# Optimization experiments

Measured on AMD Instinct MI355X. Metric: run time of the kernel, lower is better.

## Reference

```python
import jax, jax.numpy as jnp
import numpy as np

N_NODES = 100000
N_EDGES = 1600000
N_GRAPHS = 256
D = 128
L = 3
N_OUT = 10


def setup_inputs() -> dict:
    key = jax.random.key(0)
    ks = jax.random.split(key, 6)
    x = jax.random.normal(ks[0], (N_NODES, D), dtype=jnp.float32)
    edge_index = jax.random.randint(ks[1], (2, N_EDGES), 0, N_NODES, dtype=jnp.int64)
    batch = jnp.sort(jax.random.randint(ks[2], (N_NODES,), 0, N_GRAPHS, dtype=jnp.int64))
    conv_w = jax.random.normal(ks[3], (L, D, D), dtype=jnp.float32) * (1.0 / np.sqrt(D))
    conv_b = jnp.zeros((L, D), dtype=jnp.float32)
    out_w = jax.random.normal(ks[4], (3 * D, N_OUT), dtype=jnp.float32) * (1.0 / np.sqrt(3 * D))
    out_b = jnp.zeros((N_OUT,), dtype=jnp.float32)
    return {"x": x, "edge_index": edge_index, "batch": batch,
            "conv_w": conv_w, "conv_b": conv_b, "out_w": out_w, "out_b": out_b}


def reference(x, edge_index, batch, conv_w, conv_b, out_w, out_b):
    N = x.shape[0]
    # --- add self-loops (PyG GCNConv default) ---
    loop = jnp.arange(N, dtype=edge_index.dtype)
    src = jnp.concatenate([edge_index[0], loop])  # [E+N]
    dst = jnp.concatenate([edge_index[1], loop])
    # --- symmetric normalization: deg computed on dst (col) ---
    deg = jax.ops.segment_sum(jnp.ones_like(dst, dtype=x.dtype), dst, num_segments=N)
    dinv = jnp.where(deg > 0, jax.lax.rsqrt(jnp.maximum(deg, 1.0)), 0.0)
    norm = dinv[src] * dinv[dst]  # [E+N]

    h = x
    for l in range(conv_w.shape[0]):
        h = h @ conv_w[l]                                   # [N, D] transform first
        msg = h[src] * norm[:, None]                        # gather + scale
        h = jax.ops.segment_sum(msg, dst, num_segments=N)   # scatter-add
        h = jax.nn.relu(h + conv_b[l])

    # --- global max / mean / add pooling over graphs ---
    B = N_GRAPHS
    gmax = jax.ops.segment_max(h, batch, num_segments=B)
    gsum = jax.ops.segment_sum(h, batch, num_segments=B)
    cnt = jax.ops.segment_sum(jnp.ones((N, 1), h.dtype), batch, num_segments=B)
    gmean = gsum / jnp.maximum(cnt, 1.0)
    pooled = jnp.concatenate([gmax, gmean, gsum], axis=1)   # [B, 3D]
    # dropout p=0.5 is identity in eval mode
    return pooled @ out_w + out_b
```

## Files before the change

### kernel.cpp

```cpp
#include <hip/hip_runtime.h>
#include <hip/hip_bf16.h>

#define D 128
#define NP 8
#define DPB 64
#define KPB (DPB * NP)
#define SUB 64
#define CAP_SUB 64

typedef __attribute__((ext_vector_type(8))) __bf16 bf16x8;
typedef __attribute__((ext_vector_type(4))) float f32x4;
typedef __attribute__((ext_vector_type(4))) short s16x4;
typedef __attribute__((ext_vector_type(8))) short s16x8;

static __device__ __forceinline__ short f2bf(float f) {
    union { float f; unsigned u; } in; in.f = f;
    unsigned u = in.u;
    u += 0x7fffu + ((u >> 16) & 1u);
    return (short)(u >> 16);
}

__global__ void k_bucket(const int* __restrict__ src, const int* __restrict__ dst,
                         int* __restrict__ bcnt, int* __restrict__ staging,
                         int E, int KBE) {
    int i = blockIdx.x * 256 + threadIdx.x;
    if (i >= E) return;
    int d = dst[i], s = src[i];
    int b = d >> 6;
    int key = ((d & 63) << 3) | (s >> 14);
    int j = blockIdx.x & (SUB - 1);
    int slot = atomicAdd(&bcnt[j * KBE + b], 1);
    if (slot < CAP_SUB) staging[((size_t)j * KBE + b) * CAP_SUB + slot] = (key << 17) | s;
}

__global__ void k_btot(const int* __restrict__ bcnt, int* __restrict__ btot, int KBE) {
    int b = blockIdx.x * 256 + threadIdx.x;
    if (b >= KBE) return;
    int v = 0;
    #pragma unroll
    for (int j = 0; j < SUB; j++) {
        int c = bcnt[j * KBE + b];
        v += (c > CAP_SUB) ? CAP_SUB : c;
    }
    btot[b] = v;
}

__global__ void k_bscan(const int* __restrict__ btot, int* __restrict__ bbase,
                        int* __restrict__ row_ptr, int nkeys, int KBE) {
    __shared__ int sm[512];
    __shared__ int carry;
    int t = threadIdx.x;
    if (t == 0) carry = 0;
    __syncthreads();
    for (int c0 = 0; c0 < KBE; c0 += 512) {
        int b = c0 + t;
        int v = (b < KBE) ? btot[b] : 0;
        sm[t] = v;
        __syncthreads();
        for (int off = 1; off < 512; off <<= 1) {
            int x = (t >= off) ? sm[t - off] : 0;
            __syncthreads();
            sm[t] += x;
            __syncthreads();
        }
        if (b < KBE) bbase[b] = sm[t] - v + carry;
        __syncthreads();
        if (t == 0) carry += sm[511];
        __syncthreads();
    }
    if (t == 0) { bbase[KBE] = carry; row_ptr[nkeys] = carry; }
}

__global__ __launch_bounds__(256) void k_build(
    const int* __restrict__ staging, const int* __restrict__ bcnt,
    const int* __restrict__ bbase, int* __restrict__ row_ptr,
    int* __restrict__ csr_src, float* __restrict__ dinv, int N, int KBE)
{
    const int b = blockIdx.x;
    const int tid = threadIdx.x;
    __shared__ int cnt[KPB];
    __shared__ int subn[SUB];
    __shared__ int chunkbuf[256];
    __shared__ int carry;

    if (tid < SUB) {
        int c = bcnt[tid * KBE + b];
        subn[tid] = (c > CAP_SUB) ? CAP_SUB : c;
    }
    for (int k = tid; k < KPB; k += 256) cnt[k] = 0;
    if (tid == 0) carry = 0;
    __syncthreads();

    const int base = bbase[b];
    const int nb = bbase[b + 1] - base;
    const int j = tid >> 2, l4 = tid & 3;
    const int* __restrict__ sreg = staging + ((size_t)j * KBE + b) * CAP_SUB;
    const int sn = subn[j];

    for (int e = l4; e < sn; e += 4)
        atomicAdd(&cnt[sreg[e] >> 17], 1);
    __syncthreads();

    #pragma unroll 1
    for (int c = 0; c < KPB / 256; c++) {
        int idx = c * 256 + tid;
        int v = cnt[idx];
        chunkbuf[tid] = v;
        __syncthreads();
        for (int off = 1; off < 256; off <<= 1) {
            int x = (tid >= off) ? chunkbuf[tid - off] : 0;
            __syncthreads();
            chunkbuf[tid] += x;
            __syncthreads();
        }
        cnt[idx] = chunkbuf[tid] - v + carry;
        __syncthreads();
        if (tid == 255) carry += chunkbuf[255];
        __syncthreads();
    }

    for (int k = tid; k < KPB; k += 256)
        row_ptr[(size_t)b * KPB + k] = base + cnt[k];
    for (int dl = tid; dl < DPB; dl += 256) {
        int d = b * DPB + dl;
        if (d < N) {
            int hi2 = (dl == DPB - 1) ? nb : cnt[(dl + 1) * NP];
            int deg = hi2 - cnt[dl * NP];
            dinv[d] = rsqrtf((float)deg + 1.0f);
        }
    }
    __syncthreads();

    for (int e = l4; e < sn; e += 4) {
        int w = sreg[e];
        int slot = base + atomicAdd(&cnt[w >> 17], 1);
        csr_src[slot] = w & 0x1FFFF;
    }
}

__global__ void k_gseg(const int* __restrict__ batch, int* __restrict__ gstart,
                       int* __restrict__ gcnt, int N, int B) {
    int g = blockIdx.x * blockDim.x + threadIdx.x;
    if (g > B) return;
    int lo = 0, hi = N;
    while (lo < hi) {
        int mid = (lo + hi) >> 1;
        if (batch[mid] < g) lo = mid + 1; else hi = mid;
    }
    gstart[g] = lo;
    if (g < B) {
        int lo2 = lo, hi2 = N;
        while (lo2 < hi2) {
            int mid = (lo2 + hi2) >> 1;
            if (batch[mid] < g + 1) lo2 = mid + 1; else hi2 = mid;
        }
        gcnt[g] = lo2 - lo;
    }
}

__global__ void k_cvt_x(const float* __restrict__ x, const float* __restrict__ dinv,
                        short* __restrict__ xb, int total4) {
    int i = blockIdx.x * blockDim.x + threadIdx.x;
    if (i < total4) {
        float d = dinv[i >> 5];
        float4 v = ((const float4*)x)[i];
        s16x4 o;
        o.x = f2bf(v.x * d); o.y = f2bf(v.y * d);
        o.z = f2bf(v.z * d); o.w = f2bf(v.w * d);
        ((s16x4*)xb)[i] = o;
    }
}

__global__ void k_cvt_w(const float* __restrict__ W, short* __restrict__ Wt, int total) {
    int i = blockIdx.x * blockDim.x + threadIdx.x;
    if (i < total) {
        int l = i >> 14;
        int rem = i & 16383;
        int n = rem >> 7;
        int k = rem & 127;
        Wt[i] = f2bf(W[(l << 14) + (k << 7) + n]);
    }
}

__global__ __launch_bounds__(256) void k_layer(
    const short* __restrict__ hin, const int* __restrict__ row_ptr,
    const int* __restrict__ csr_src, const float* __restrict__ dinv,
    const short* __restrict__ Wt, const float* __restrict__ bias,
    short* __restrict__ hout, float* __restrict__ hrelu, int N, int mode)
{
    __shared__ __align__(16) short tile[16 * 128];
    const int tid = threadIdx.x;
    const int wave = tid >> 6;
    const int lane = tid & 63;
    const int group = lane >> 4;
    const int lg = lane & 15;
    const int off = lg * 8;
    const int node_base = blockIdx.x * 16;
    const int r = wave * 4 + group;
    const int i = node_base + r;

    short* dstp = &tile[r * 128 + ((lg ^ (r & 7)) << 3)];
    if (i < N) {
        float acc[8];
        bf16x8 v = *(const bf16x8*)(hin + (size_t)i * D + off);
        #pragma unroll
        for (int k = 0; k < 8; k++) acc[k] = (float)v[k];

        int t = row_ptr[i * NP];
        const int end = row_ptr[i * NP + NP];
        const int nfull = (end - t) >> 3;

        int i0, i1, i2, i3, i4, i5, i6, i7;
        if (nfull > 0) {
            i0 = csr_src[t + 0]; i1 = csr_src[t + 1];
            i2 = csr_src[t + 2]; i3 = csr_src[t + 3];
            i4 = csr_src[t + 4]; i5 = csr_src[t + 5];
            i6 = csr_src[t + 6]; i7 = csr_src[t + 7];
        }
        #pragma unroll 1
        for (int c = 0; c < nfull; c++) {
            bf16x8 v0 = *(const bf16x8*)(hin + (size_t)i0 * D + off);
            bf16x8 v1 = *(const bf16x8*)(hin + (size_t)i1 * D + off);
            bf16x8 v2 = *(const bf16x8*)(hin + (size_t)i2 * D + off);
            bf16x8 v3 = *(const bf16x8*)(hin + (size_t)i3 * D + off);
            bf16x8 v4 = *(const bf16x8*)(hin + (size_t)i4 * D + off);
            bf16x8 v5 = *(const bf16x8*)(hin + (size_t)i5 * D + off);
            bf16x8 v6 = *(const bf16x8*)(hin + (size_t)i6 * D + off);
            bf16x8 v7 = *(const bf16x8*)(hin + (size_t)i7 * D + off);
            t += 8;
            if (c + 1 < nfull) {
                i0 = csr_src[t + 0]; i1 = csr_src[t + 1];
                i2 = csr_src[t + 2]; i3 = csr_src[t + 3];
                i4 = csr_src[t + 4]; i5 = csr_src[t + 5];
                i6 = csr_src[t + 6]; i7 = csr_src[t + 7];
            }
            #pragma unroll
            for (int k = 0; k < 8; k++)
                acc[k] += ((((float)v0[k] + (float)v1[k]) + ((float)v2[k] + (float)v3[k]))
                         + (((float)v4[k] + (float)v5[k]) + ((float)v6[k] + (float)v7[k])));
        }
        for (; t + 4 <= end; t += 4) {
            int j0 = csr_src[t + 0], j1 = csr_src[t + 1];
            int j2 = csr_src[t + 2], j3 = csr_src[t + 3];
            bf16x8 v0 = *(const bf16x8*)(hin + (size_t)j0 * D + off);
            bf16x8 v1 = *(const bf16x8*)(hin + (size_t)j1 * D + off);
            bf16x8 v2 = *(const bf16x8*)(hin + (size_t)j2 * D + off);
            bf16x8 v3 = *(const bf16x8*)(hin + (size_t)j3 * D + off);
            #pragma unroll
            for (int k = 0; k < 8; k++)
                acc[k] += (((float)v0[k] + (float)v1[k]) + ((float)v2[k] + (float)v3[k]));
        }
        for (; t < end; t++) {
            int j0 = csr_src[t];
            bf16x8 v0 = *(const bf16x8*)(hin + (size_t)j0 * D + off);
            #pragma unroll
            for (int k = 0; k < 8; k++) acc[k] += (float)v0[k];
        }

        const float di = dinv[i];
        s16x8 o;
        #pragma unroll
        for (int k = 0; k < 8; k++) o[k] = f2bf(acc[k] * di);
        *(s16x8*)dstp = o;
    } else {
        s16x8 z = {0, 0, 0, 0, 0, 0, 0, 0};
        *(s16x8*)dstp = z;
    }
    __syncthreads();

    bf16x8 afrag[4];
    #pragma unroll
    for (int kt = 0; kt < 4; kt++)
        afrag[kt] = *(const bf16x8*)(&tile[lg * 128 + (((group + 4 * kt) ^ (lg & 7)) << 3)]);

    f32x4 acc2[2];
    #pragma unroll
    for (int nt = 0; nt < 2; nt++) { f32x4 z = {0.f, 0.f, 0.f, 0.f}; acc2[nt] = z; }
    #pragma unroll
    for (int nt = 0; nt < 2; nt++) {
        const short* bp = Wt + (size_t)(wave * 32 + nt * 16 + lg) * D + group * 8;
        #pragma unroll
        for (int kt = 0; kt < 4; kt++) {
            bf16x8 b = *(const bf16x8*)(bp + kt * 32);
            acc2[nt] = __builtin_amdgcn_mfma_f32_16x16x32_bf16(afrag[kt], b, acc2[nt], 0, 0, 0);
        }
    }

    float bcol[2];
    #pragma unroll
    for (int nt = 0; nt < 2; nt++) bcol[nt] = bias[wave * 32 + nt * 16 + lg];
    const int row0 = node_base + group * 4;
    #pragma unroll
    for (int i2 = 0; i2 < 4; i2++) {
        int r2 = row0 + i2;
        if (r2 < N) {
            if (mode == 0) {
                float dr = dinv[r2];
                #pragma unroll
                for (int nt = 0; nt < 2; nt++) {
                    int col = wave * 32 + nt * 16 + lg;
                    float val = fmaxf(acc2[nt][i2] + bcol[nt], 0.0f);
                    hout[(size_t)r2 * D + col] = f2bf(val * dr);
                }
            } else {
                #pragma unroll
                for (int nt = 0; nt < 2; nt++) {
                    int col = wave * 32 + nt * 16 + lg;
                    hrelu[(size_t)r2 * D + col] = fmaxf(acc2[nt][i2] + bcol[nt], 0.0f);
                }
            }
        }
    }
}

__global__ __launch_bounds__(256) void k_pool(const float* __restrict__ hrelu,
                                              const int* __restrict__ gstart,
                                              const int* __restrict__ gcnt,
                                              float* __restrict__ pmax,
                                              float* __restrict__ psum, int B) {
    int g = blockIdx.x >> 2;
    int q = blockIdx.x & 3;
    int c = threadIdx.x & 127;
    int p = threadIdx.x >> 7;
    int start = gstart[g];
    int endr = start + gcnt[g];

    float mx0 = 0.f, mx1 = 0.f, sm0 = 0.f, sm1 = 0.f;
    int r = start + q * 2 + p;
    for (; r + 8 < endr; r += 16) {
        float v0 = hrelu[(size_t)r * D + c];
        float v1 = hrelu[(size_t)(r + 8) * D + c];
        mx0 = fmaxf(mx0, v0); sm0 += v0;
        mx1 = fmaxf(mx1, v1); sm1 += v1;
    }
    if (r < endr) {
        float v0 = hrelu[(size_t)r * D + c];
        mx0 = fmaxf(mx0, v0); sm0 += v0;
    }
    float mx = fmaxf(mx0, mx1), sm = sm0 + sm1;

    __shared__ float smx[128], ssm[128];
    if (p == 1) { smx[c] = mx; ssm[c] = sm; }
    __syncthreads();
    if (p == 0) {
        pmax[((size_t)q * B + g) * D + c] = fmaxf(mx, smx[c]);
        psum[((size_t)q * B + g) * D + c] = sm + ssm[c];
    }
}

__global__ void k_final(const float* __restrict__ pmax, const float* __restrict__ psum,
                        const int* __restrict__ gcnt, const float* __restrict__ ow,
                        const float* __restrict__ ob, float* __restrict__ out, int B) {
    int g = blockIdx.x;
    int t = threadIdx.x;
    float part[10];
    #pragma unroll
    for (int o = 0; o < 10; o++) part[o] = 0.f;
    float invc = 1.0f / fmaxf((float)gcnt[g], 1.0f);
    for (int k = t; k < 3 * D; k += 64) {
        int c = (k < D) ? k : ((k < 2 * D) ? k - D : k - 2 * D);
        float pk;
        if (k < D) {
            float m = pmax[(size_t)g * D + c];
            #pragma unroll
            for (int q = 1; q < 4; q++) m = fmaxf(m, pmax[((size_t)q * B + g) * D + c]);
            pk = m;
        } else {
            float s = psum[(size_t)g * D + c];
            #pragma unroll
            for (int q = 1; q < 4; q++) s += psum[((size_t)q * B + g) * D + c];
            pk = (k < 2 * D) ? s * invc : s;
        }
        const float* w = ow + k * 10;
        #pragma unroll
        for (int o = 0; o < 10; o++) part[o] += pk * w[o];
    }
    #pragma unroll
    for (int off = 32; off > 0; off >>= 1)
        #pragma unroll
        for (int o = 0; o < 10; o++) part[o] += __shfl_down(part[o], off, 64);
    if (t == 0)
        #pragma unroll
        for (int o = 0; o < 10; o++) out[g * 10 + o] = part[o] + ob[o];
}

extern "C" void kernel_launch(void* const* d_in, const int* in_sizes, int n_in,
                              void* d_out, int out_size, void* d_ws, size_t ws_size,
                              hipStream_t stream) {
    const float* x     = (const float*)d_in[0];
    const int*   ei    = (const int*)d_in[1];
    const int*   batch = (const int*)d_in[2];
    const float* convw = (const float*)d_in[3];
    const float* convb = (const float*)d_in[4];
    const float* outw  = (const float*)d_in[5];
    const float* outb  = (const float*)d_in[6];
    float* out = (float*)d_out;

    const int N = in_sizes[0] / D;
    const int E = in_sizes[1] / 2;
    const int L = in_sizes[3] / (D * D);
    const int B = out_size / 10;

    const int* src = ei;
    const int* dst = ei + E;

    const int KBE   = (N + DPB - 1) / DPB;
    const int nkeys = KBE * KPB;

    char* p = (char*)d_ws;
    auto alloc = [&](size_t bytes) { char* r = p; p += (bytes + 255) & ~255ull; return r; };
    short* hb0     = (short*)alloc((size_t)N * D * 2);
    short* hb1     = (short*)alloc((size_t)N * D * 2);
    float* hrelu   = (float*)alloc((size_t)N * D * 4);
    short* Wt      = (short*)alloc((size_t)L * D * D * 2);
    int*   row_ptr = (int*)alloc(((size_t)nkeys + 1) * 4);
    int*   csr_src = (int*)alloc((size_t)E * 4);
    int*   bcnt    = (int*)alloc((size_t)SUB * KBE * 4);
    int*   btot    = (int*)alloc((size_t)KBE * 4);
    int*   bbase   = (int*)alloc(((size_t)KBE + 1) * 4);
    float* dinv    = (float*)alloc((size_t)N * 4);
    float* pmax    = (float*)alloc((size_t)4 * B * D * 4);
    float* psum    = (float*)alloc((size_t)4 * B * D * 4);
    int*   gcnt    = (int*)alloc((size_t)B * 4);
    int*   gstart  = (int*)alloc(((size_t)B + 1) * 4);

    int* staging = (int*)hrelu;

    hipMemsetAsync(bcnt, 0, (size_t)SUB * KBE * 4, stream);

    k_bucket<<<(E + 255) / 256, 256, 0, stream>>>(src, dst, bcnt, staging, E, KBE);
    k_gseg<<<1, 512, 0, stream>>>(batch, gstart, gcnt, N, B);
    k_btot<<<(KBE + 255) / 256, 256, 0, stream>>>(bcnt, btot, KBE);
    k_bscan<<<1, 512, 0, stream>>>(btot, bbase, row_ptr, nkeys, KBE);
    k_build<<<KBE, 256, 0, stream>>>(staging, bcnt, bbase, row_ptr, csr_src, dinv, N, KBE);
    k_cvt_x<<<((N * D / 4) + 255) / 256, 256, 0, stream>>>(x, dinv, hb0, N * D / 4);
    k_cvt_w<<<((L * D * D) + 255) / 256, 256, 0, stream>>>(convw, Wt, L * D * D);

    const int lblocks = (N + 15) / 16;
    k_layer<<<lblocks, 256, 0, stream>>>(hb0, row_ptr, csr_src, dinv, Wt,
                                         convb, hb1, hrelu, N, 0);
    k_layer<<<lblocks, 256, 0, stream>>>(hb1, row_ptr, csr_src, dinv, Wt + D * D,
                                         convb + D, hb0, hrelu, N, 0);
    k_layer<<<lblocks, 256, 0, stream>>>(hb0, row_ptr, csr_src, dinv, Wt + 2 * D * D,
                                         convb + 2 * D, hb1, hrelu, N, 1);

    k_pool<<<B * 4, 256, 0, stream>>>(hrelu, gstart, gcnt, pmax, psum, B);
    k_final<<<B, 64, 0, stream>>>(pmax, psum, gcnt, outw, outb, out, B);
}
```

Measured before the change: 458.1 us.

## Merge setup kernels, use wave-shuffle scans, add nontemporal loads

Folds the weight conversion and graph-segment search into the bucketing kernel, and merges the per-bucket total into the single-block scan. Both scans (bucket offsets and per-block CSR offsets) switch from LDS Hillis-Steele loops with many barriers to wave shuffle scans. Nontemporal loads are added for edge indices, x and the pooling reads. The aim is fewer launches and fewer barriers in the preprocessing stages. In exchange the single-block scan now does the 64-way bcnt reduction serially per thread.

New measurement: 454.0 us. About the same (-0.9%).

```diff
diff --git a/kernel.cpp b/kernel.cpp
--- a/kernel.cpp
+++ b/kernel.cpp
@@ -22,53 +22,90 @@
 
 __global__ void k_bucket(const int* __restrict__ src, const int* __restrict__ dst,
                          int* __restrict__ bcnt, int* __restrict__ staging,
-                         int E, int KBE) {
-    int i = blockIdx.x * 256 + threadIdx.x;
-    if (i >= E) return;
-    int d = dst[i], s = src[i];
-    int b = d >> 6;
-    int key = ((d & 63) << 3) | (s >> 14);
-    int j = blockIdx.x & (SUB - 1);
-    int slot = atomicAdd(&bcnt[j * KBE + b], 1);
-    if (slot < CAP_SUB) staging[((size_t)j * KBE + b) * CAP_SUB + slot] = (key << 17) | s;
-}
-
-__global__ void k_btot(const int* __restrict__ bcnt, int* __restrict__ btot, int KBE) {
-    int b = blockIdx.x * 256 + threadIdx.x;
-    if (b >= KBE) return;
-    int v = 0;
-    #pragma unroll
-    for (int j = 0; j < SUB; j++) {
-        int c = bcnt[j * KBE + b];
-        v += (c > CAP_SUB) ? CAP_SUB : c;
-    }
-    btot[b] = v;
-}
-
-__global__ void k_bscan(const int* __restrict__ btot, int* __restrict__ bbase,
+                         int E, int KBE,
+                         const float* __restrict__ W, short* __restrict__ Wt, int totw,
+                         const int* __restrict__ batch, int* __restrict__ gstart,
+                         int* __restrict__ gcnt, int N, int B) {
+    const int EB = (E + 255) >> 8;
+    if (blockIdx.x < (unsigned)EB) {
+        int i = blockIdx.x * 256 + threadIdx.x;
+        if (i >= E) return;
+        int d = __builtin_nontemporal_load(dst + i);
+        int s = __builtin_nontemporal_load(src + i);
+        int b = d >> 6;
+        int key = ((d & 63) << 3) | (s >> 14);
+        int j = blockIdx.x & (SUB - 1);
+        int slot = atomicAdd(&bcnt[j * KBE + b], 1);
+        if (slot < CAP_SUB) staging[((size_t)j * KBE + b) * CAP_SUB + slot] = (key << 17) | s;
+    } else if ((int)blockIdx.x - EB < (totw >> 8)) {
+        int i = (blockIdx.x - EB) * 256 + threadIdx.x;
+        if (i < totw) {
+            int l = i >> 14;
+            int rem = i & 16383;
+            int n = rem >> 7;
+            int k = rem & 127;
+            Wt[i] = f2bf(W[(l << 14) + (k << 7) + n]);
+        }
+    } else {
+        for (int g = threadIdx.x; g <= B; g += 256) {
+            int lo = 0, hi = N;
+            while (lo < hi) {
+                int mid = (lo + hi) >> 1;
+                if (batch[mid] < g) lo = mid + 1; else hi = mid;
+            }
+            gstart[g] = lo;
+            if (g < B) {
+                int lo2 = lo, hi2 = N;
+                while (lo2 < hi2) {
+                    int mid = (lo2 + hi2) >> 1;
+                    if (batch[mid] < g + 1) lo2 = mid + 1; else hi2 = mid;
+                }
+                gcnt[g] = lo2 - lo;
+            }
+        }
+    }
+}
+
+__global__ void k_bscan(const int* __restrict__ bcnt, int* __restrict__ bbase,
                         int* __restrict__ row_ptr, int nkeys, int KBE) {
-    __shared__ int sm[512];
-    __shared__ int carry;
-    int t = threadIdx.x;
-    if (t == 0) carry = 0;
+    __shared__ int wtot[8];
+    __shared__ int carry_s;
+    const int t = threadIdx.x;
+    const int w = t >> 6;
+    const int lane = t & 63;
+    if (t == 0) carry_s = 0;
     __syncthreads();
     for (int c0 = 0; c0 < KBE; c0 += 512) {
-        int b = c0 + t;
-        int v = (b < KBE) ? btot[b] : 0;
-        sm[t] = v;
-        __syncthreads();
-        for (int off = 1; off < 512; off <<= 1) {
-            int x = (t >= off) ? sm[t - off] : 0;
-            __syncthreads();
-            sm[t] += x;
-            __syncthreads();
-        }
-        if (b < KBE) bbase[b] = sm[t] - v + carry;
-        __syncthreads();
-        if (t == 0) carry += sm[511];
-        __syncthreads();
-    }
-    if (t == 0) { bbase[KBE] = carry; row_ptr[nkeys] = carry; }
+        const int b = c0 + t;
+        int v = 0;
+        if (b < KBE) {
+            #pragma unroll 8
+            for (int j = 0; j < SUB; j++) {
+                int c = bcnt[j * KBE + b];
+                v += (c > CAP_SUB) ? CAP_SUB : c;
+            }
+        }
+        int is = v;
+        #pragma unroll
+        for (int off = 1; off < 64; off <<= 1) {
+            int x = __shfl_up(is, off, 64);
+            if (lane >= off) is += x;
+        }
+        if (lane == 63) wtot[w] = is;
+        __syncthreads();
+        if (t == 0) {
+            int run = 0;
+            #pragma unroll
+            for (int i = 0; i < 8; i++) { int x = wtot[i]; wtot[i] = run; run += x; }
+        }
+        __syncthreads();
+        const int excl = is - v + wtot[w] + carry_s;
+        if (b < KBE) bbase[b] = excl;
+        __syncthreads();
+        if (t == 511) carry_s = excl + v;
+        __syncthreads();
+    }
+    if (t == 0) { bbase[KBE] = carry_s; row_ptr[nkeys] = carry_s; }
 }
 
 __global__ __launch_bounds__(256) void k_build(
@@ -80,15 +117,13 @@
     const int tid = threadIdx.x;
     __shared__ int cnt[KPB];
     __shared__ int subn[SUB];
-    __shared__ int chunkbuf[256];
-    __shared__ int carry;
+    __shared__ int wtot[4];
 
     if (tid < SUB) {
         int c = bcnt[tid * KBE + b];
         subn[tid] = (c > CAP_SUB) ? CAP_SUB : c;
     }
     for (int k = tid; k < KPB; k += 256) cnt[k] = 0;
-    if (tid == 0) carry = 0;
     __syncthreads();
 
     const int base = bbase[b];
@@ -101,21 +136,27 @@
         atomicAdd(&cnt[sreg[e] >> 17], 1);
     __syncthreads();
 
-    #pragma unroll 1
-    for (int c = 0; c < KPB / 256; c++) {
-        int idx = c * 256 + tid;
-        int v = cnt[idx];
-        chunkbuf[tid] = v;
-        __syncthreads();
-        for (int off = 1; off < 256; off <<= 1) {
-            int x = (tid >= off) ? chunkbuf[tid - off] : 0;
-            __syncthreads();
-            chunkbuf[tid] += x;
-            __syncthreads();
-        }
-        cnt[idx] = chunkbuf[tid] - v + carry;
-        __syncthreads();
-        if (tid == 255) carry += chunkbuf[255];
+    {
+        const int w = tid >> 6, lane = tid & 63;
+        const int e0 = cnt[2 * tid], e1 = cnt[2 * tid + 1];
+        const int s = e0 + e1;
+        int is = s;
+        #pragma unroll
+        for (int off = 1; off < 64; off <<= 1) {
+            int x = __shfl_up(is, off, 64);
+            if (lane >= off) is += x;
+        }
+        if (lane == 63) wtot[w] = is;
+        __syncthreads();
+        if (tid == 0) {
+            int run = 0;
+            #pragma unroll
+            for (int i = 0; i < 4; i++) { int x = wtot[i]; wtot[i] = run; run += x; }
+        }
+        __syncthreads();
+        const int excl = is - s + wtot[w];
+        cnt[2 * tid] = excl;
+        cnt[2 * tid + 1] = excl + e0;
         __syncthreads();
     }
 
@@ -138,47 +179,16 @@
     }
 }
 
-__global__ void k_gseg(const int* __restrict__ batch, int* __restrict__ gstart,
-                       int* __restrict__ gcnt, int N, int B) {
-    int g = blockIdx.x * blockDim.x + threadIdx.x;
-    if (g > B) return;
-    int lo = 0, hi = N;
-    while (lo < hi) {
-        int mid = (lo + hi) >> 1;
-        if (batch[mid] < g) lo = mid + 1; else hi = mid;
-    }
-    gstart[g] = lo;
-    if (g < B) {
-        int lo2 = lo, hi2 = N;
-        while (lo2 < hi2) {
-            int mid = (lo2 + hi2) >> 1;
-            if (batch[mid] < g + 1) lo2 = mid + 1; else hi2 = mid;
-        }
-        gcnt[g] = lo2 - lo;
-    }
-}
-
 __global__ void k_cvt_x(const float* __restrict__ x, const float* __restrict__ dinv,
                         short* __restrict__ xb, int total4) {
     int i = blockIdx.x * blockDim.x + threadIdx.x;
     if (i < total4) {
         float d = dinv[i >> 5];
-        float4 v = ((const float4*)x)[i];
+        f32x4 v = __builtin_nontemporal_load((const f32x4*)x + i);
         s16x4 o;
         o.x = f2bf(v.x * d); o.y = f2bf(v.y * d);
         o.z = f2bf(v.z * d); o.w = f2bf(v.w * d);
         ((s16x4*)xb)[i] = o;
-    }
-}
-
-__global__ void k_cvt_w(const float* __restrict__ W, short* __restrict__ Wt, int total) {
-    int i = blockIdx.x * blockDim.x + threadIdx.x;
-    if (i < total) {
-        int l = i >> 14;
-        int rem = i & 16383;
-        int n = rem >> 7;
-        int k = rem & 127;
-        Wt[i] = f2bf(W[(l << 14) + (k << 7) + n]);
     }
 }
 
@@ -328,13 +338,13 @@
     float mx0 = 0.f, mx1 = 0.f, sm0 = 0.f, sm1 = 0.f;
     int r = start + q * 2 + p;
     for (; r + 8 < endr; r += 16) {
-        float v0 = hrelu[(size_t)r * D + c];
-        float v1 = hrelu[(size_t)(r + 8) * D + c];
+        float v0 = __builtin_nontemporal_load(hrelu + (size_t)r * D + c);
+        float v1 = __builtin_nontemporal_load(hrelu + (size_t)(r + 8) * D + c);
         mx0 = fmaxf(mx0, v0); sm0 += v0;
         mx1 = fmaxf(mx1, v1); sm1 += v1;
     }
     if (r < endr) {
-        float v0 = hrelu[(size_t)r * D + c];
+        float v0 = __builtin_nontemporal_load(hrelu + (size_t)r * D + c);
         mx0 = fmaxf(mx0, v0); sm0 += v0;
     }
     float mx = fmaxf(mx0, mx1), sm = sm0 + sm1;
@@ -406,6 +416,8 @@
 
     const int KBE   = (N + DPB - 1) / DPB;
     const int nkeys = KBE * KPB;
+    const int totw  = L * D * D;
+    const int EB    = (E + 255) / 256;
 
     char* p = (char*)d_ws;
     auto alloc = [&](size_t bytes) { char* r = p; p += (bytes + 255) & ~255ull; return r; };
@@ -416,7 +428,6 @@
     int*   row_ptr = (int*)alloc(((size_t)nkeys + 1) * 4);
     int*   csr_src = (int*)alloc((size_t)E * 4);
     int*   bcnt    = (int*)alloc((size_t)SUB * KBE * 4);
-    int*   btot    = (int*)alloc((size_t)KBE * 4);
     int*   bbase   = (int*)alloc(((size_t)KBE + 1) * 4);
     float* dinv    = (float*)alloc((size_t)N * 4);
     float* pmax    = (float*)alloc((size_t)4 * B * D * 4);
@@ -428,13 +439,12 @@
 
     hipMemsetAsync(bcnt, 0, (size_t)SUB * KBE * 4, stream);
 
-    k_bucket<<<(E + 255) / 256, 256, 0, stream>>>(src, dst, bcnt, staging, E, KBE);
-    k_gseg<<<1, 512, 0, stream>>>(batch, gstart, gcnt, N, B);
-    k_btot<<<(KBE + 255) / 256, 256, 0, stream>>>(bcnt, btot, KBE);
-    k_bscan<<<1, 512, 0, stream>>>(btot, bbase, row_ptr, nkeys, KBE);
+    k_bucket<<<EB + totw / 256 + 1, 256, 0, stream>>>(src, dst, bcnt, staging, E, KBE,
+                                                      convw, Wt, totw,
+                                                      batch, gstart, gcnt, N, B);
+    k_bscan<<<1, 512, 0, stream>>>(bcnt, bbase, row_ptr, nkeys, KBE);
     k_build<<<KBE, 256, 0, stream>>>(staging, bcnt, bbase, row_ptr, csr_src, dinv, N, KBE);
     k_cvt_x<<<((N * D / 4) + 255) / 256, 256, 0, stream>>>(x, dinv, hb0, N * D / 4);
-    k_cvt_w<<<((L * D * D) + 255) / 256, 256, 0, stream>>>(convw, Wt, L * D * D);
 
     const int lblocks = (N + 15) / 16;
     k_layer<<<lblocks, 256, 0, stream>>>(hb0, row_ptr, csr_src, dinv, Wt,
```
